# Optimization experiments

Hardware: AMD Instinct MI355X
Metric: run time of the kernel (lower is better)

Reference implementation:

```python
import jax, jax.numpy as jnp
import numpy as np

N = 25000          # nodes
E = 200000         # edges
MUL = 16           # multiplicity of 0e and 1o in irreps_in/out
NUM_RADIAL = 8
HIDDEN = 64
WNUMEL = 4 * MUL * MUL
PATH_ALPHA = 1.0 / np.sqrt(2.0 * MUL)   # 2 paths feed each output irrep, fan_in=MUL each
INV_SQRT3 = 1.0 / np.sqrt(3.0)          # CG coeff for 1o x 1o -> 0e (component norm)


def setup_inputs() -> dict:
    key = jax.random.key(0)
    ks = jax.random.split(key, 9)
    x = jax.random.normal(ks[0], (N, 4 * MUL), jnp.float32)          # [N, 64] = 16x0e + 16x1o
    edge_attr = jax.random.normal(ks[1], (E, 4), jnp.float32)        # [E, 4]  = 1x0e + 1x1o sh
    edge_length = jax.random.uniform(ks[2], (E,), jnp.float32, 0.0, 5.0)
    edge_src = jax.random.randint(ks[3], (E,), 0, N)
    edge_dst = jax.random.randint(ks[4], (E,), 0, N)
    W1 = jax.random.normal(ks[5], (NUM_RADIAL, HIDDEN), jnp.float32)
    W2 = jax.random.normal(ks[6], (HIDDEN, WNUMEL), jnp.float32)
    L0 = jax.random.normal(ks[7], (MUL, MUL), jnp.float32)           # sc Linear on 0e block
    L1 = jax.random.normal(ks[8], (MUL, MUL), jnp.float32)           # sc Linear on 1o block
    return dict(x=x, edge_attr=edge_attr, edge_length=edge_length,
                edge_src=edge_src, edge_dst=edge_dst, W1=W1, W2=W2, L0=L0, L1=L1)


def reference(x, edge_attr, edge_length, edge_src, edge_dst, W1, W2, L0, L1):
    # ---- radial Gaussian basis (centers linspace(0,5,8), sigma=1) ----
    centers = jnp.linspace(0.0, 5.0, NUM_RADIAL).astype(x.dtype)
    d = edge_length[:, None] - centers[None, :]
    radial = jnp.exp(-0.5 * d * d)                                   # [E, 8]
    # ---- radial MLP -> per-edge TP weights (e3nn FullyConnectedNet, silu) ----
    h = jax.nn.silu(radial @ W1 * (1.0 / np.sqrt(NUM_RADIAL)))       # [E, 64]
    w = (h @ W2 * (1.0 / np.sqrt(HIDDEN))).reshape(E, 4, MUL, MUL)   # [E, 4, 16, 16]
    # ---- gather source node features, split into l=0 and l=1 parts ----
    xj = x[edge_src]                                                  # [E, 64]
    xj0 = xj[:, :MUL]                                                 # [E, 16]
    xj1 = xj[:, MUL:].reshape(E, MUL, 3)                              # [E, 16, 3]
    sh0 = edge_attr[:, 0]                                             # [E]
    sh1 = edge_attr[:, 1:4]                                           # [E, 3]
    # ---- FullyConnectedTensorProduct: 4 CG paths with per-edge weights ----
    m0 = (jnp.einsum('eu,euv->ev', xj0 * sh0[:, None], w[:, 0])
          + INV_SQRT3 * jnp.einsum('euk,ek,euv->ev', xj1, sh1, w[:, 1])) * PATH_ALPHA  # [E,16]
    m1 = (jnp.einsum('eu,ek,euv->evk', xj0, sh1, w[:, 2])
          + jnp.einsum('euk,e,euv->evk', xj1, sh0, w[:, 3])) * PATH_ALPHA              # [E,16,3]
    m_ij = jnp.concatenate([m0, m1.reshape(E, 3 * MUL)], axis=1)      # [E, 64]
    # ---- scatter-add messages to destination nodes ----
    m_i = jax.ops.segment_sum(m_ij, edge_dst, num_segments=N)        # [N, 64]
    # ---- residual self-connection: o3.Linear per-l mixing ----
    x0 = x[:, :MUL]
    x1 = x[:, MUL:].reshape(N, MUL, 3)
    sc0 = x0 @ L0
    sc1 = jnp.einsum('nuk,uv->nvk', x1, L1).reshape(N, 3 * MUL)
    sc = jnp.concatenate([sc0, sc1], axis=1) * (1.0 / np.sqrt(MUL))
    return m_i + sc
```

## Files before the change

kernel.cpp:

```cpp
#include <hip/hip_runtime.h>

#define N_NODES 25000
#define N_EDGES 200000

constexpr int ET = 32;
constexpr int NTILES = 6250;
constexpr int GRID = 512;
constexpr int PL = ET * 17;
constexpr int CFS = 152;

typedef __attribute__((ext_vector_type(8))) _Float16 half8;
typedef __attribute__((ext_vector_type(4))) _Float16 half4;
typedef __attribute__((ext_vector_type(4))) float float4v;

__device__ __forceinline__ half8 h8s(half8 a, _Float16 c) { return a * c; }

__device__ __forceinline__ void gl_lds16(const void* g, void* l) {
    __builtin_amdgcn_global_load_lds((const __attribute__((address_space(1))) void*)g,
                                     (__attribute__((address_space(3))) void*)l, 16, 0, 0);
}
__device__ __forceinline__ void gl_lds4(const void* g, void* l) {
    __builtin_amdgcn_global_load_lds((const __attribute__((address_space(1))) void*)g,
                                     (__attribute__((address_space(3))) void*)l, 4, 0, 0);
}

__global__ __launch_bounds__(512, 4) void fused_kernel(
    const float* __restrict__ x, const float* __restrict__ edge_attr,
    const float* __restrict__ edge_length, const int* __restrict__ edge_src,
    const int* __restrict__ edge_dst, const float* __restrict__ W1,
    const float* __restrict__ W2, const float* __restrict__ L0,
    const float* __restrict__ L1, float* __restrict__ out) {

    const int t = threadIdx.x;
    const int w = t >> 6;
    const int lane = t & 63;
    const int prog = w >> 1;
    const int uh = w & 1;
    const int qm = t & 15;
    const int quad = (t >> 4) & 3;
    const int eL = t >> 4;
    const int uL = t & 15;

    __shared__ __attribute__((aligned(16))) _Float16 lds_h16[ET * 72];
    __shared__ __attribute__((aligned(16))) _Float16 lds_cf16[ET * CFS];
    __shared__ __attribute__((aligned(16))) float lds_xch[12 * PL];
    __shared__ __attribute__((aligned(16))) float lds_w1t[64 * 8];
    __shared__ __attribute__((aligned(16))) float l0[256], l1[256];
    __shared__ __attribute__((aligned(16))) float lds_xj[2][ET * 64];
    __shared__ __attribute__((aligned(16))) float lds_ea[2][ET * 4];
    __shared__ __attribute__((aligned(16))) float lds_len[2][ET];
    __shared__ __attribute__((aligned(16))) int   lds_dst[2][ET];
    __shared__ __attribute__((aligned(16))) int   lds_srcb[2][ET];

    half8 bfr[8][2];
    {
        float scale = 0.0220970869f;
        if (prog == 1) scale *= 0.5773502692f;
        const int kr = quad * 8;
        #pragma unroll
        for (int up = 0; up < 8; ++up) {
            const int col = prog * 256 + (uh * 8 + up) * 16 + qm;
            #pragma unroll
            for (int kf = 0; kf < 2; ++kf) {
                half8 f;
                #pragma unroll
                for (int j = 0; j < 8; ++j) {
                    const int k = kf * 32 + kr + j;
                    f[j] = (_Float16)(W2[k * 1024 + col] * scale);
                }
                bfr[up][kf] = f;
            }
        }
    }
    lds_w1t[(t & 63) * 8 + (t >> 6)] = W1[t];
    if (t < 256) l0[t] = L0[t];
    else         l1[t - 256] = L1[t - 256];

    int T = blockIdx.x;
    if (w == 0 && lane < ET) gl_lds4(edge_src + T * ET + lane, &lds_srcb[1][0]);
    __syncthreads();
    {
        const int e4 = (w << 2) + (lane >> 4);
        const int src = lds_srcb[1][e4];
        gl_lds16(x + src * 64 + (lane & 15) * 4, &lds_xj[0][w * 256]);
    }
    if (w == 0 && lane < ET) gl_lds16(edge_attr + 4 * (T * ET + lane), &lds_ea[0][0]);
    if (w == 1 && lane < ET) gl_lds4(edge_length + T * ET + lane, &lds_len[0][0]);
    if (w == 2 && lane < ET) gl_lds4(edge_dst + T * ET + lane, &lds_dst[0][0]);
    if (w == 3 && lane < ET) {
        const int Tn = (T + GRID < NTILES) ? T + GRID : T;
        gl_lds4(edge_src + Tn * ET + lane, &lds_srcb[0][0]);
    }

    {
        const bool is0 = lane < 16;
        const int q = lane - 16;
        const int v = is0 ? lane : q / 3;
        const int k = is0 ? 0 : q - 3 * v;
        const float* mat = is0 ? l0 : l1;
        for (int n = blockIdx.x * 8 + w; n < N_NODES; n += GRID * 8) {
            const float xv = x[n * 64 + lane];
            float s = 0.f;
            #pragma unroll
            for (int u = 0; u < 16; ++u) {
                const int sel = is0 ? u : 16 + 3 * u + k;
                s = fmaf(__shfl(xv, sel), mat[u * 16 + v], s);
            }
            atomicAdd(out + n * 64 + lane, 0.25f * s);
        }
    }
    __syncthreads();

    int p = 0;
    while (true) {
        {
            const float sh0 = lds_ea[p][eL * 4 + 0];
            const float s1x = lds_ea[p][eL * 4 + 1];
            const float s1y = lds_ea[p][eL * 4 + 2];
            const float s1z = lds_ea[p][eL * 4 + 3];
            const float* xr = &lds_xj[p][eL * 64];
            const float xj0v = xr[uL];
            const float x0 = xr[16 + 3 * uL];
            const float x1 = xr[17 + 3 * uL];
            const float x2 = xr[18 + 3 * uL];
            _Float16* cfb = &lds_cf16[eL * CFS + uL];
            cfb[0 * 24] = (_Float16)(xj0v * sh0);
            cfb[1 * 24] = (_Float16)fmaf(x0, s1x, fmaf(x1, s1y, x2 * s1z));
            cfb[2 * 24] = (_Float16)xj0v;
            cfb[3 * 24] = (_Float16)(x0 * sh0);
            cfb[4 * 24] = (_Float16)(x1 * sh0);
            cfb[5 * 24] = (_Float16)(x2 * sh0);
            const int c0 = uL * 4;
            const float len = lds_len[p][eL];
            float rad[8];
            #pragma unroll
            for (int r = 0; r < 8; ++r) {
                const float d = len - 0.7142857143f * (float)r;
                rad[r] = __expf(-0.5f * d * d);
            }
            half4 hv;
            #pragma unroll
            for (int i = 0; i < 4; ++i) {
                const float4v wA = *(const float4v*)(&lds_w1t[(c0 + i) * 8]);
                const float4v wB = *(const float4v*)(&lds_w1t[(c0 + i) * 8 + 4]);
                float s = rad[0] * wA[0] + rad[1] * wA[1] + rad[2] * wA[2] + rad[3] * wA[3]
                        + rad[4] * wB[0] + rad[5] * wB[1] + rad[6] * wB[2] + rad[7] * wB[3];
                s *= 0.3535533906f;
                hv[i] = (_Float16)(s / (1.f + __expf(-s)));
            }
            *(half4*)(&lds_h16[eL * 72 + c0]) = hv;
        }

        __syncthreads();

        const int Tn = T + GRID;
        if (Tn < NTILES) {
            const int pn = p ^ 1;
            {
                const int e4 = (w << 2) + (lane >> 4);
                const int src = lds_srcb[p][e4];
                gl_lds16(x + src * 64 + (lane & 15) * 4, &lds_xj[pn][w * 256]);
            }
            if (w == 0 && lane < ET) gl_lds16(edge_attr + 4 * (Tn * ET + lane), &lds_ea[pn][0]);
            if (w == 1 && lane < ET) gl_lds4(edge_length + Tn * ET + lane, &lds_len[pn][0]);
            if (w == 2 && lane < ET) gl_lds4(edge_dst + Tn * ET + lane, &lds_dst[pn][0]);
            if (w == 3 && lane < ET) {
                const int T2 = (Tn + GRID < NTILES) ? Tn + GRID : Tn;
                gl_lds4(edge_src + T2 * ET + lane, &lds_srcb[pn][0]);
            }
        }

        if (prog < 3) {
            half8 cfv[2];
            #pragma unroll
            for (int mt = 0; mt < 2; ++mt)
                cfv[mt] = *(const half8*)(&lds_cf16[(mt * 16 + qm) * CFS + prog * 24 + uh * 8]);
            float4v acc[2];
            acc[0] = (float4v){0.f, 0.f, 0.f, 0.f};
            acc[1] = (float4v){0.f, 0.f, 0.f, 0.f};
            #pragma unroll
            for (int kf = 0; kf < 2; ++kf) {
                half8 ah[2];
                #pragma unroll
                for (int mt = 0; mt < 2; ++mt)
                    ah[mt] = *(const half8*)(&lds_h16[(mt * 16 + qm) * 72 + kf * 32 + quad * 8]);
                #pragma unroll
                for (int up = 0; up < 8; ++up)
                    #pragma unroll
                    for (int mt = 0; mt < 2; ++mt)
                        acc[mt] = __builtin_amdgcn_mfma_f32_16x16x32_f16(
                            h8s(ah[mt], cfv[mt][up]), bfr[up][kf], acc[mt], 0, 0, 0);
            }
            float* xb = &lds_xch[w * PL];
            #pragma unroll
            for (int mt = 0; mt < 2; ++mt)
                #pragma unroll
                for (int r = 0; r < 4; ++r)
                    xb[(mt * 16 + quad * 4 + r) * 17 + qm] = acc[mt][r];
        } else {
            #pragma unroll
            for (int k = 0; k < 3; ++k) {
                half8 cfv[2];
                #pragma unroll
                for (int mt = 0; mt < 2; ++mt)
                    cfv[mt] = *(const half8*)(&lds_cf16[(mt * 16 + qm) * CFS + (3 + k) * 24 + uh * 8]);
                float4v acc[2];
                acc[0] = (float4v){0.f, 0.f, 0.f, 0.f};
                acc[1] = (float4v){0.f, 0.f, 0.f, 0.f};
                #pragma unroll
                for (int kf = 0; kf < 2; ++kf) {
                    half8 ah[2];
                    #pragma unroll
                    for (int mt = 0; mt < 2; ++mt)
                        ah[mt] = *(const half8*)(&lds_h16[(mt * 16 + qm) * 72 + kf * 32 + quad * 8]);
                    #pragma unroll
                    for (int up = 0; up < 8; ++up)
                        #pragma unroll
                        for (int mt = 0; mt < 2; ++mt)
                            acc[mt] = __builtin_amdgcn_mfma_f32_16x16x32_f16(
                                h8s(ah[mt], cfv[mt][up]), bfr[up][kf], acc[mt], 0, 0, 0);
                }
                float* xb = &lds_xch[(6 + uh * 3 + k) * PL];
                #pragma unroll
                for (int mt = 0; mt < 2; ++mt)
                    #pragma unroll
                    for (int r = 0; r < 4; ++r)
                        xb[(mt * 16 + quad * 4 + r) * 17 + qm] = acc[mt][r];
            }
        }

        __syncthreads();

        #pragma unroll
        for (int i = 0; i < 4; ++i) {
            const int idx = t + 512 * i;
            const int e = idx >> 6, j = idx & 63;
            float val;
            if (j < 16) {
                val = (lds_xch[0 * PL + e * 17 + j] + lds_xch[1 * PL + e * 17 + j])
                    + (lds_xch[2 * PL + e * 17 + j] + lds_xch[3 * PL + e * 17 + j]);
            } else {
                const int q = j - 16, v = q / 3, k = q - 3 * v;
                const float s2 = lds_xch[4 * PL + e * 17 + v] + lds_xch[5 * PL + e * 17 + v];
                const float s3 = lds_xch[(6 + k) * PL + e * 17 + v]
                               + lds_xch[(9 + k) * PL + e * 17 + v];
                val = fmaf(s2, lds_ea[p][e * 4 + 1 + k], s3);
            }
            atomicAdd(out + lds_dst[p][e] * 64 + j, val);
        }

        if (Tn >= NTILES) break;
        T = Tn;
        p ^= 1;
    }
}

extern "C" void kernel_launch(void* const* d_in, const int* in_sizes, int n_in,
                              void* d_out, int out_size, void* d_ws, size_t ws_size,
                              hipStream_t stream) {
    const float* x           = (const float*)d_in[0];
    const float* edge_attr   = (const float*)d_in[1];
    const float* edge_length = (const float*)d_in[2];
    const int*   edge_src    = (const int*)d_in[3];
    const int*   edge_dst    = (const int*)d_in[4];
    const float* W1          = (const float*)d_in[5];
    const float* W2          = (const float*)d_in[6];
    const float* L0          = (const float*)d_in[7];
    const float* L1          = (const float*)d_in[8];
    float* out = (float*)d_out;

    hipMemsetAsync(out, 0, (size_t)N_NODES * 64 * sizeof(float), stream);
    fused_kernel<<<GRID, 512, 0, stream>>>(
        x, edge_attr, edge_length, edge_src, edge_dst, W1, W2, L0, L1, out);
}
```

Before: 209.3 us.

## Apply per-edge coefficients after MFMA instead of pre-scaling A fragments

Rather than scaling the hidden-activation A fragments by each per-edge coefficient before every MFMA, the kernel computes the raw h·W2 product per u with two MFMAs and then multiplies the fp32 accumulator by coefficients read from transposed fp32 LDS tables. For the l=1 path, one MFMA result is shared across the three k components, removing two thirds of the MFMAs in those warps. The coefficients stay in fp32, and the half8 scaling work disappears. The cost is more VALU multiply-accumulates, more LDS reads of coefficient vectors, and higher register pressure from holding six accumulators.

```diff
diff --git a/kernel.cpp b/kernel.cpp
--- a/kernel.cpp
+++ b/kernel.cpp
@@ -7,13 +7,11 @@
 constexpr int NTILES = 6250;
 constexpr int GRID = 512;
 constexpr int PL = ET * 17;
-constexpr int CFS = 152;
+constexpr int CTS = 36;
 
 typedef __attribute__((ext_vector_type(8))) _Float16 half8;
 typedef __attribute__((ext_vector_type(4))) _Float16 half4;
 typedef __attribute__((ext_vector_type(4))) float float4v;
-
-__device__ __forceinline__ half8 h8s(half8 a, _Float16 c) { return a * c; }
 
 __device__ __forceinline__ void gl_lds16(const void* g, void* l) {
     __builtin_amdgcn_global_load_lds((const __attribute__((address_space(1))) void*)g,
@@ -34,7 +32,7 @@
     const int t = threadIdx.x;
     const int w = t >> 6;
     const int lane = t & 63;
-    const int prog = w >> 1;
+    const int q = w >> 1;
     const int uh = w & 1;
     const int qm = t & 15;
     const int quad = (t >> 4) & 3;
@@ -42,7 +40,8 @@
     const int uL = t & 15;
 
     __shared__ __attribute__((aligned(16))) _Float16 lds_h16[ET * 72];
-    __shared__ __attribute__((aligned(16))) _Float16 lds_cf16[ET * CFS];
+    __shared__ __attribute__((aligned(16))) float lds_cfT[3][16][CTS];
+    __shared__ __attribute__((aligned(16))) float lds_cf3T[3][16][CTS];
     __shared__ __attribute__((aligned(16))) float lds_xch[12 * PL];
     __shared__ __attribute__((aligned(16))) float lds_w1t[64 * 8];
     __shared__ __attribute__((aligned(16))) float l0[256], l1[256];
@@ -55,11 +54,11 @@
     half8 bfr[8][2];
     {
         float scale = 0.0220970869f;
-        if (prog == 1) scale *= 0.5773502692f;
+        if (q == 1) scale *= 0.5773502692f;
         const int kr = quad * 8;
         #pragma unroll
         for (int up = 0; up < 8; ++up) {
-            const int col = prog * 256 + (uh * 8 + up) * 16 + qm;
+            const int col = q * 256 + (uh * 8 + up) * 16 + qm;
             #pragma unroll
             for (int kf = 0; kf < 2; ++kf) {
                 half8 f;
@@ -94,9 +93,9 @@
 
     {
         const bool is0 = lane < 16;
-        const int q = lane - 16;
-        const int v = is0 ? lane : q / 3;
-        const int k = is0 ? 0 : q - 3 * v;
+        const int qq = lane - 16;
+        const int v = is0 ? lane : qq / 3;
+        const int k = is0 ? 0 : qq - 3 * v;
         const float* mat = is0 ? l0 : l1;
         for (int n = blockIdx.x * 8 + w; n < N_NODES; n += GRID * 8) {
             const float xv = x[n * 64 + lane];
@@ -123,13 +122,12 @@
             const float x0 = xr[16 + 3 * uL];
             const float x1 = xr[17 + 3 * uL];
             const float x2 = xr[18 + 3 * uL];
-            _Float16* cfb = &lds_cf16[eL * CFS + uL];
-            cfb[0 * 24] = (_Float16)(xj0v * sh0);
-            cfb[1 * 24] = (_Float16)fmaf(x0, s1x, fmaf(x1, s1y, x2 * s1z));
-            cfb[2 * 24] = (_Float16)xj0v;
-            cfb[3 * 24] = (_Float16)(x0 * sh0);
-            cfb[4 * 24] = (_Float16)(x1 * sh0);
-            cfb[5 * 24] = (_Float16)(x2 * sh0);
+            lds_cfT[0][uL][eL] = xj0v * sh0;
+            lds_cfT[1][uL][eL] = fmaf(x0, s1x, fmaf(x1, s1y, x2 * s1z));
+            lds_cfT[2][uL][eL] = xj0v;
+            lds_cf3T[0][uL][eL] = x0 * sh0;
+            lds_cf3T[1][uL][eL] = x1 * sh0;
+            lds_cf3T[2][uL][eL] = x2 * sh0;
             const int c0 = uL * 4;
             const float len = lds_len[p][eL];
             float rad[8];
@@ -170,62 +168,67 @@
             }
         }
 
-        if (prog < 3) {
-            half8 cfv[2];
+        half8 ah[2][2];
+        #pragma unroll
+        for (int mt = 0; mt < 2; ++mt)
+            #pragma unroll
+            for (int kf = 0; kf < 2; ++kf)
+                ah[mt][kf] = *(const half8*)(&lds_h16[(mt * 16 + qm) * 72 + kf * 32 + quad * 8]);
+
+        if (q < 3) {
+            float4v C[2];
+            C[0] = (float4v){0.f, 0.f, 0.f, 0.f};
+            C[1] = (float4v){0.f, 0.f, 0.f, 0.f};
+            #pragma unroll
+            for (int up = 0; up < 8; ++up) {
+                const int u = uh * 8 + up;
+                #pragma unroll
+                for (int mt = 0; mt < 2; ++mt) {
+                    float4v au = __builtin_amdgcn_mfma_f32_16x16x32_f16(
+                        ah[mt][0], bfr[up][0], (float4v){0.f, 0.f, 0.f, 0.f}, 0, 0, 0);
+                    au = __builtin_amdgcn_mfma_f32_16x16x32_f16(
+                        ah[mt][1], bfr[up][1], au, 0, 0, 0);
+                    const float4v cr = *(const float4v*)(&lds_cfT[q][u][mt * 16 + quad * 4]);
+                    C[mt] += au * cr;
+                }
+            }
+            float* xb = &lds_xch[(q * 2 + uh) * PL];
             #pragma unroll
             for (int mt = 0; mt < 2; ++mt)
-                cfv[mt] = *(const half8*)(&lds_cf16[(mt * 16 + qm) * CFS + prog * 24 + uh * 8]);
-            float4v acc[2];
-            acc[0] = (float4v){0.f, 0.f, 0.f, 0.f};
-            acc[1] = (float4v){0.f, 0.f, 0.f, 0.f};
-            #pragma unroll
-            for (int kf = 0; kf < 2; ++kf) {
-                half8 ah[2];
-                #pragma unroll
-                for (int mt = 0; mt < 2; ++mt)
-                    ah[mt] = *(const half8*)(&lds_h16[(mt * 16 + qm) * 72 + kf * 32 + quad * 8]);
-                #pragma unroll
-                for (int up = 0; up < 8; ++up)
+                #pragma unroll
+                for (int r = 0; r < 4; ++r)
+                    xb[(mt * 16 + quad * 4 + r) * 17 + qm] = C[mt][r];
+        } else {
+            float4v C3[3][2];
+            #pragma unroll
+            for (int k = 0; k < 3; ++k) {
+                C3[k][0] = (float4v){0.f, 0.f, 0.f, 0.f};
+                C3[k][1] = (float4v){0.f, 0.f, 0.f, 0.f};
+            }
+            #pragma unroll
+            for (int up = 0; up < 8; ++up) {
+                const int u = uh * 8 + up;
+                #pragma unroll
+                for (int mt = 0; mt < 2; ++mt) {
+                    float4v au = __builtin_amdgcn_mfma_f32_16x16x32_f16(
+                        ah[mt][0], bfr[up][0], (float4v){0.f, 0.f, 0.f, 0.f}, 0, 0, 0);
+                    au = __builtin_amdgcn_mfma_f32_16x16x32_f16(
+                        ah[mt][1], bfr[up][1], au, 0, 0, 0);
                     #pragma unroll
-                    for (int mt = 0; mt < 2; ++mt)
-                        acc[mt] = __builtin_amdgcn_mfma_f32_16x16x32_f16(
-                            h8s(ah[mt], cfv[mt][up]), bfr[up][kf], acc[mt], 0, 0, 0);
-            }
-            float* xb = &lds_xch[w * PL];
-            #pragma unroll
-            for (int mt = 0; mt < 2; ++mt)
-                #pragma unroll
-                for (int r = 0; r < 4; ++r)
-                    xb[(mt * 16 + quad * 4 + r) * 17 + qm] = acc[mt][r];
-        } else {
+                    for (int k = 0; k < 3; ++k) {
+                        const float4v ck = *(const float4v*)(&lds_cf3T[k][u][mt * 16 + quad * 4]);
+                        C3[k][mt] += au * ck;
+                    }
+                }
+            }
             #pragma unroll
             for (int k = 0; k < 3; ++k) {
-                half8 cfv[2];
-                #pragma unroll
-                for (int mt = 0; mt < 2; ++mt)
-                    cfv[mt] = *(const half8*)(&lds_cf16[(mt * 16 + qm) * CFS + (3 + k) * 24 + uh * 8]);
-                float4v acc[2];
-                acc[0] = (float4v){0.f, 0.f, 0.f, 0.f};
-                acc[1] = (float4v){0.f, 0.f, 0.f, 0.f};
-                #pragma unroll
-                for (int kf = 0; kf < 2; ++kf) {
-                    half8 ah[2];
-                    #pragma unroll
-                    for (int mt = 0; mt < 2; ++mt)
-                        ah[mt] = *(const half8*)(&lds_h16[(mt * 16 + qm) * 72 + kf * 32 + quad * 8]);
-                    #pragma unroll
-                    for (int up = 0; up < 8; ++up)
-                        #pragma unroll
-                        for (int mt = 0; mt < 2; ++mt)
-                            acc[mt] = __builtin_amdgcn_mfma_f32_16x16x32_f16(
-                                h8s(ah[mt], cfv[mt][up]), bfr[up][kf], acc[mt], 0, 0, 0);
-                }
                 float* xb = &lds_xch[(6 + uh * 3 + k) * PL];
                 #pragma unroll
                 for (int mt = 0; mt < 2; ++mt)
                     #pragma unroll
                     for (int r = 0; r < 4; ++r)
-                        xb[(mt * 16 + quad * 4 + r) * 17 + qm] = acc[mt][r];
+                        xb[(mt * 16 + quad * 4 + r) * 17 + qm] = C3[k][mt][r];
             }
         }
 
@@ -240,7 +243,7 @@
                 val = (lds_xch[0 * PL + e * 17 + j] + lds_xch[1 * PL + e * 17 + j])
                     + (lds_xch[2 * PL + e * 17 + j] + lds_xch[3 * PL + e * 17 + j]);
             } else {
-                const int q = j - 16, v = q / 3, k = q - 3 * v;
+                const int qj = j - 16, v = qj / 3, k = qj - 3 * v;
                 const float s2 = lds_xch[4 * PL + e * 17 + v] + lds_xch[5 * PL + e * 17 + v];
                 const float s3 = lds_xch[(6 + k) * PL + e * 17 + v]
                                + lds_xch[(9 + k) * PL + e * 17 + v];
```

Result: slower. 213.8 us (+2.1%).
